# Kernel optimization log

Hardware: AMD Instinct MI355X
Metric: run time of the kernel (lower is better)

Reference implementation:

```python
import jax, jax.numpy as jnp
import numpy as np

E, TOPK = 8, 2
N_EMBD, TEXT_DIM, FULL = 1024, 1024, 1024
BS, SEQ = 8, 512

def setup_inputs() -> dict:
    key = jax.random.key(0)
    ks = jax.random.split(key, 8)
    return {
        "x": jax.random.normal(ks[0], (BS, SEQ, N_EMBD), jnp.float32),
        "dec_embeddings": jax.random.normal(ks[1], (BS, TEXT_DIM), jnp.float32),
        # router is zero-init in the module, but use small random weights so top-k is non-degenerate
        "router_w": jax.random.normal(ks[2], (E, TEXT_DIM), jnp.float32) * 0.02,
        "router_b": jnp.zeros((E,), jnp.float32),
        "w1": jax.random.normal(ks[3], (E, N_EMBD, N_EMBD), jnp.float32) * 0.02,
        "w2": jax.random.normal(ks[4], (E, N_EMBD, FULL), jnp.float32) * 0.02,
        "b1": jnp.zeros((E, 1, N_EMBD), jnp.float32),
        "b2": jnp.zeros((E, 1, FULL), jnp.float32),
    }

def reference(x, dec_embeddings, router_w, router_b, w1, w2, b1, b2):
    bs, seqlen, n_embd = x.shape
    logits = dec_embeddings @ router_w.T + router_b          # (bs, E)
    gate_probs = jax.nn.softmax(logits, axis=-1)
    topk_w, topk_idx = jax.lax.top_k(gate_probs, TOPK)       # (bs, k)
    topk_w = topk_w / jnp.sum(topk_w, axis=-1, keepdims=True)
    # dense all-expert 2-layer MLP (as written in the original)
    hidden = jax.nn.relu(jnp.einsum('bsn,enh->ebsh', x, w1) + b1[:, None])   # (E,bs,S,H)
    out_all = jnp.einsum('ebsh,ehf->ebsf', hidden, w2) + b2[:, None]          # (E,bs,S,F)
    out_b = jnp.transpose(out_all, (1, 0, 2, 3))             # (bs,E,S,F)
    # gather top-k expert outputs per batch item and combine
    sel = jnp.take_along_axis(out_b, topk_idx[:, :, None, None], axis=1)      # (bs,k,S,F)
    final_output = jnp.sum(topk_w[:, :, None, None] * sel, axis=1)            # (bs,S,F)
    combined_mask = jnp.max(jax.nn.one_hot(topk_idx, E, dtype=x.dtype), axis=1)  # (bs,E)
    aux_loss = E * jnp.sum(jnp.mean(gate_probs, axis=0) * jnp.mean(combined_mask, axis=0))
    return final_output, aux_loss, combined_mask, logits
```

## Files before the change

kernel.cpp:

```cpp
#include <hip/hip_runtime.h>
#include <hip/hip_bf16.h>
#include <stdint.h>

#define EXP 8
#define DIM 1024
#define SEQL 512
#define BATCH 8
#define OUT_FINAL_N (BATCH * SEQL * DIM)
#define OFF_AUX    4194304
#define OFF_MASK   4194305
#define OFF_LOGITS 4194369

typedef __bf16 bf16_t;
typedef bf16_t bf16x8 __attribute__((ext_vector_type(8)));
typedef bf16_t bf16x4 __attribute__((ext_vector_type(4)));
typedef float  f32x4  __attribute__((ext_vector_type(4)));

typedef __attribute__((address_space(1))) void* as1p;
typedef __attribute__((address_space(3))) void* as3p;

__device__ __forceinline__ void glds16(const void* g, void* l) {
  __builtin_amdgcn_global_load_lds((as1p)(void*)g, (as3p)l, 16, 0, 0);
}

__global__ __launch_bounds__(256) void prep_kernel(
    const float* __restrict__ x, const float* __restrict__ dec,
    const float* __restrict__ rw, const float* __restrict__ rb,
    const float* __restrict__ w1, const float* __restrict__ w2,
    bf16_t* __restrict__ xb, bf16_t* __restrict__ w1t, bf16_t* __restrict__ w2t,
    float* __restrict__ out_aux, float* __restrict__ out_mask,
    float* __restrict__ out_logits, int* __restrict__ idx_ws,
    float* __restrict__ w_ws) {
  __shared__ __align__(16) char tileb[64 * 144];
  __shared__ float part[256];
  __shared__ float lg64[64];
  __shared__ float probs[64];
  __shared__ float msk[64];
  const int bid = blockIdx.x;
  const int t = threadIdx.x;

  if (bid < 4096) {
    const int z = bid >> 8;
    const int rem = bid & 255;
    const int k0 = (rem >> 4) * 64;
    const int n0 = (rem & 15) * 64;
    const float* src = (z < 8) ? (w1 + (size_t)z * DIM * DIM)
                               : (w2 + (size_t)(z - 8) * DIM * DIM);
    bf16_t* dst = (z < 8) ? (w1t + (size_t)z * DIM * DIM)
                          : (w2t + (size_t)(z - 8) * DIM * DIM);
    const int c4 = t & 15;
    const int rr = t >> 4;
    float4 v[4];
#pragma unroll
    for (int r = 0; r < 4; ++r)
      v[r] = *(const float4*)(src + (size_t)(k0 + rr * 4 + r) * DIM + n0 + c4 * 4);
    const float* vp = (const float*)v;
#pragma unroll
    for (int c = 0; c < 4; ++c) {
      bf16x4 o;
#pragma unroll
      for (int jk = 0; jk < 4; ++jk) o[jk] = (bf16_t)vp[jk * 4 + c];
      *(bf16x4*)(tileb + (c4 * 4 + c) * 144 + rr * 8) = o;
    }
    __syncthreads();
#pragma unroll
    for (int ii = 0; ii < 2; ++ii) {
      const int n = (t >> 3) + 32 * ii;
      const int j = t & 7;
      bf16x8 vv = *(const bf16x8*)(tileb + n * 144 + j * 16);
      *(bf16x8*)(dst + (size_t)(n0 + n) * DIM + k0 + j * 8) = vv;
    }
  } else if (bid < 4096 + 512) {
    const int i0 = (bid - 4096) * 2048 + t;
    float4 v[8];
#pragma unroll
    for (int i = 0; i < 8; ++i) v[i] = ((const float4*)x)[i0 + i * 256];
#pragma unroll
    for (int i = 0; i < 8; ++i) {
      bf16x4 o;
      o[0] = (bf16_t)v[i].x; o[1] = (bf16_t)v[i].y;
      o[2] = (bf16_t)v[i].z; o[3] = (bf16_t)v[i].w;
      ((bf16x4*)xb)[i0 + i * 256] = o;
    }
  } else {
    const int p = t >> 2, seg = t & 3;
    const int b = p >> 3, e = p & 7;
    const float4* dv = (const float4*)(dec + b * DIM + seg * 256);
    const float4* wv = (const float4*)(rw + e * DIM + seg * 256);
    float s = 0.f;
#pragma unroll 8
    for (int i = 0; i < 64; ++i) {
      float4 a = dv[i], c = wv[i];
      s += a.x * c.x + a.y * c.y + a.z * c.z + a.w * c.w;
    }
    part[t] = s;
    __syncthreads();
    if (seg == 0) {
      float l = part[t] + part[t + 1] + part[t + 2] + part[t + 3] + rb[e];
      lg64[p] = l;
      out_logits[p] = l;
    }
    __syncthreads();
    if (t < 8) {
      float l[8];
      float mx = -1e30f;
#pragma unroll
      for (int k = 0; k < 8; ++k) { l[k] = lg64[t * 8 + k]; mx = fmaxf(mx, l[k]); }
      float pe[8];
      float sum = 0.f;
#pragma unroll
      for (int k = 0; k < 8; ++k) { pe[k] = expf(l[k] - mx); sum += pe[k]; }
      float inv = 1.f / sum;
#pragma unroll
      for (int k = 0; k < 8; ++k) { pe[k] *= inv; probs[t * 8 + k] = pe[k]; }
      int i0 = 0;
#pragma unroll
      for (int k = 1; k < 8; ++k) if (pe[k] > pe[i0]) i0 = k;
      int i1 = (i0 == 0) ? 1 : 0;
#pragma unroll
      for (int k = 0; k < 8; ++k) if (k != i0 && pe[k] > pe[i1]) i1 = k;
      float p0 = pe[i0], p1 = pe[i1];
      float invs = 1.f / (p0 + p1);
      idx_ws[t * 2] = i0;
      idx_ws[t * 2 + 1] = i1;
      w_ws[t * 2] = p0 * invs;
      w_ws[t * 2 + 1] = p1 * invs;
#pragma unroll
      for (int k = 0; k < 8; ++k) {
        float m = (k == i0 || k == i1) ? 1.f : 0.f;
        msk[t * 8 + k] = m;
        out_mask[t * 8 + k] = m;
      }
    }
    __syncthreads();
    if (t == 0) {
      float aux = 0.f;
#pragma unroll
      for (int k = 0; k < 8; ++k) {
        float mp = 0.f, mm = 0.f;
#pragma unroll
        for (int bb = 0; bb < 8; ++bb) { mp += probs[bb * 8 + k]; mm += msk[bb * 8 + k]; }
        aux += (mp * 0.125f) * (mm * 0.125f);
      }
      out_aux[0] = 8.f * aux;
    }
  }
}

__global__ __launch_bounds__(512, 2) void gemm1_kernel(const bf16_t* __restrict__ xb,
                                                       const bf16_t* __restrict__ w1t,
                                                       const float* __restrict__ b1,
                                                       const int* __restrict__ topk_idx,
                                                       bf16_t* __restrict__ hidden) {
  __shared__ __align__(16) char smem[73728];
  const int tid = threadIdx.x;
  const int g = tid >> 8;
  const int t = tid & 255;
  const int bN = blockIdx.x, bM = blockIdx.y, b = blockIdx.z;
  const int slot = b * 2 + g;
  const int e = topk_idx[slot];

  const bf16_t* A  = xb + ((size_t)b * SEQL + bM * 128) * DIM;
  const bf16_t* Bt = w1t + ((size_t)e * DIM + bN * 128) * DIM;

  char* sA = smem;
  char* sB = smem + 24576 + g * 24576;

  const int rlA = tid >> 2, cpA = (tid & 3) ^ (rlA & 3);
  const bf16_t* gA = A + (size_t)rlA * DIM + cpA * 8;
  const int rlB = t >> 2, cpB = (t & 3) ^ (rlB & 3);
  const bf16_t* gB0 = Bt + (size_t)rlB * DIM + cpB * 8;
  const bf16_t* gB1 = gB0 + (size_t)64 * DIM;

  const int lane = tid & 63, wg = (tid >> 6) & 3;
  const int wr = wg >> 1, wc = wg & 1;
  const int m15 = lane & 15, q = lane >> 4;
  const char* ra[4];
  const char* rb[4];
#pragma unroll
  for (int i = 0; i < 4; ++i) {
    const int r = wr * 64 + i * 16 + m15;
    ra[i] = sA + r * 64 + ((q ^ (r & 3)) * 16);
    const int n = wc * 64 + i * 16 + m15;
    rb[i] = sB + n * 64 + ((q ^ (n & 3)) * 16);
  }

  f32x4 acc[4][4];
#pragma unroll
  for (int i = 0; i < 4; ++i)
#pragma unroll
    for (int j = 0; j < 4; ++j) acc[i][j] = {0.f, 0.f, 0.f, 0.f};

  glds16(gA, sA + tid * 16);
  glds16(gB0, sB + t * 16);
  glds16(gB1, sB + 4096 + t * 16);
  glds16(gA + 32, sA + 8192 + tid * 16);
  glds16(gB0 + 32, sB + 8192 + t * 16);
  glds16(gB1 + 32, sB + 8192 + 4096 + t * 16);

  int cur = 0;
  for (int kt = 0; kt < 32; ++kt) {
    if (kt < 31) {
      asm volatile("s_waitcnt vmcnt(3)" ::: "memory");
    } else {
      asm volatile("s_waitcnt vmcnt(0)" ::: "memory");
    }
    __builtin_amdgcn_s_barrier();
    asm volatile("" ::: "memory");
    if (kt < 30) {
      int nb = cur + 2; if (nb >= 3) nb -= 3;
      const int off = (kt + 2) * 32;
      glds16(gA + off, sA + nb * 8192 + tid * 16);
      glds16(gB0 + off, sB + nb * 8192 + t * 16);
      glds16(gB1 + off, sB + nb * 8192 + 4096 + t * 16);
    }
    bf16x8 af[4], bfr[4];
#pragma unroll
    for (int i = 0; i < 4; ++i) af[i] = *(const bf16x8*)(ra[i] + cur * 8192);
#pragma unroll
    for (int j = 0; j < 4; ++j) bfr[j] = *(const bf16x8*)(rb[j] + cur * 8192);
    __builtin_amdgcn_s_setprio(1);
#pragma unroll
    for (int i = 0; i < 4; ++i)
#pragma unroll
      for (int j = 0; j < 4; ++j)
        acc[i][j] = __builtin_amdgcn_mfma_f32_16x16x32_bf16(af[i], bfr[j], acc[i][j], 0, 0, 0);
    __builtin_amdgcn_s_setprio(0);
    cur += 1; if (cur == 3) cur = 0;
  }

  __syncthreads();
  bf16_t* hb = (bf16_t*)(smem + g * 34816);
  const float* be = b1 + e * DIM;
#pragma unroll
  for (int i = 0; i < 4; ++i)
#pragma unroll
    for (int j = 0; j < 4; ++j) {
      const int colL = wc * 64 + j * 16 + m15;
      const float bias = be[bN * 128 + colL];
#pragma unroll
      for (int r = 0; r < 4; ++r) {
        const int rowL = wr * 64 + i * 16 + q * 4 + r;
        hb[rowL * 136 + colL] = (bf16_t)fmaxf(acc[i][j][r] + bias, 0.f);
      }
    }
  __syncthreads();
  bf16_t* H = hidden + (size_t)slot * SEQL * DIM + ((size_t)bM * 128) * DIM + bN * 128;
#pragma unroll
  for (int ii = 0; ii < 8; ++ii) {
    const int r = (t >> 4) + 16 * ii;
    const int c = t & 15;
    bf16x8 vv = *(const bf16x8*)(hb + r * 136 + c * 8);
    *(bf16x8*)(H + (size_t)r * DIM + c * 8) = vv;
  }
}

__global__ __launch_bounds__(512, 2) void gemm2_kernel(const bf16_t* __restrict__ hidden,
                                                       const bf16_t* __restrict__ w2t,
                                                       const float* __restrict__ b2,
                                                       const int* __restrict__ topk_idx,
                                                       const float* __restrict__ topk_w,
                                                       float* __restrict__ out) {
  __shared__ __align__(16) char smem[98304];
  const int tid = threadIdx.x;
  const int g = tid >> 8;
  const int t = tid & 255;
  const int bN = blockIdx.x, bM = blockIdx.y, b = blockIdx.z;
  const int slot = b * 2 + g;
  const int e = topk_idx[slot];
  const float sg = topk_w[slot];

  const bf16_t* A  = hidden + ((size_t)slot * SEQL + bM * 128) * DIM;
  const bf16_t* Bt = w2t + ((size_t)e * DIM + bN * 128) * DIM;

  char* sA = smem + g * 49152;
  char* sB = sA + 24576;

  const int rl = t >> 2, cp = (t & 3) ^ (rl & 3);
  const bf16_t* gA0 = A + (size_t)rl * DIM + cp * 8;
  const bf16_t* gA1 = gA0 + (size_t)64 * DIM;
  const bf16_t* gB0 = Bt + (size_t)rl * DIM + cp * 8;
  const bf16_t* gB1 = gB0 + (size_t)64 * DIM;

  const int lane = tid & 63, wg = (tid >> 6) & 3;
  const int wr = wg >> 1, wc = wg & 1;
  const int m15 = lane & 15, q = lane >> 4;
  const char* ra[4];
  const char* rb[4];
#pragma unroll
  for (int i = 0; i < 4; ++i) {
    const int r = wr * 64 + i * 16 + m15;
    ra[i] = sA + r * 64 + ((q ^ (r & 3)) * 16);
    const int n = wc * 64 + i * 16 + m15;
    rb[i] = sB + n * 64 + ((q ^ (n & 3)) * 16);
  }

  f32x4 acc[4][4];
#pragma unroll
  for (int i = 0; i < 4; ++i)
#pragma unroll
    for (int j = 0; j < 4; ++j) acc[i][j] = {0.f, 0.f, 0.f, 0.f};

  glds16(gA0, sA + t * 16);
  glds16(gA1, sA + 4096 + t * 16);
  glds16(gB0, sB + t * 16);
  glds16(gB1, sB + 4096 + t * 16);
  glds16(gA0 + 32, sA + 8192 + t * 16);
  glds16(gA1 + 32, sA + 8192 + 4096 + t * 16);
  glds16(gB0 + 32, sB + 8192 + t * 16);
  glds16(gB1 + 32, sB + 8192 + 4096 + t * 16);

  int cur = 0;
  for (int kt = 0; kt < 32; ++kt) {
    if (kt < 31) {
      asm volatile("s_waitcnt vmcnt(4)" ::: "memory");
    } else {
      asm volatile("s_waitcnt vmcnt(0)" ::: "memory");
    }
    __builtin_amdgcn_s_barrier();
    asm volatile("" ::: "memory");
    if (kt < 30) {
      int nb = cur + 2; if (nb >= 3) nb -= 3;
      const int off = (kt + 2) * 32;
      char* dA = sA + nb * 8192 + t * 16;
      char* dB = sB + nb * 8192 + t * 16;
      glds16(gA0 + off, dA);
      glds16(gA1 + off, dA + 4096);
      glds16(gB0 + off, dB);
      glds16(gB1 + off, dB + 4096);
    }
    bf16x8 af[4], bfr[4];
#pragma unroll
    for (int i = 0; i < 4; ++i) af[i] = *(const bf16x8*)(ra[i] + cur * 8192);
#pragma unroll
    for (int j = 0; j < 4; ++j) bfr[j] = *(const bf16x8*)(rb[j] + cur * 8192);
    __builtin_amdgcn_s_setprio(1);
#pragma unroll
    for (int i = 0; i < 4; ++i)
#pragma unroll
      for (int j = 0; j < 4; ++j)
        acc[i][j] = __builtin_amdgcn_mfma_f32_16x16x32_bf16(af[i], bfr[j], acc[i][j], 0, 0, 0);
    __builtin_amdgcn_s_setprio(0);
    cur += 1; if (cur == 3) cur = 0;
  }

  __syncthreads();
  float* scr = (float*)smem;
  const float w0 = topk_w[b * 2], w1v = topk_w[b * 2 + 1];
  const float* be0 = b2 + topk_idx[b * 2] * DIM;
  const float* be1 = b2 + topk_idx[b * 2 + 1] * DIM;
  float* O = out + (size_t)b * SEQL * DIM;
#pragma unroll
  for (int i = 0; i < 4; ++i) {
    if (g == 1) {
#pragma unroll
      for (int j = 0; j < 4; ++j)
#pragma unroll
        for (int r = 0; r < 4; ++r)
          scr[(j * 4 + r) * 256 + t] = sg * acc[i][j][r];
    }
    __syncthreads();
    if (g == 0) {
#pragma unroll
      for (int j = 0; j < 4; ++j) {
        const int col = bN * 128 + wc * 64 + j * 16 + m15;
        const float bb = w0 * be0[col] + w1v * be1[col];
        const int row = bM * 128 + wr * 64 + i * 16 + q * 4;
#pragma unroll
        for (int r = 0; r < 4; ++r)
          O[(size_t)(row + r) * DIM + col] =
              sg * acc[i][j][r] + scr[(j * 4 + r) * 256 + t] + bb;
      }
    }
    __syncthreads();
  }
}

extern "C" void kernel_launch(void* const* d_in, const int* in_sizes, int n_in,
                              void* d_out, int out_size, void* d_ws, size_t ws_size,
                              hipStream_t stream) {
  const float* x   = (const float*)d_in[0];
  const float* dec = (const float*)d_in[1];
  const float* rw  = (const float*)d_in[2];
  const float* rb  = (const float*)d_in[3];
  const float* w1  = (const float*)d_in[4];
  const float* w2  = (const float*)d_in[5];
  const float* b1  = (const float*)d_in[6];
  const float* b2  = (const float*)d_in[7];
  float* out = (float*)d_out;

  char* ws = (char*)d_ws;
  bf16_t* xb   = (bf16_t*)(ws);
  bf16_t* w1t  = (bf16_t*)(ws + (8u << 20));
  bf16_t* w2t  = (bf16_t*)(ws + (24u << 20));
  bf16_t* hid  = (bf16_t*)(ws + (40u << 20));
  int*    idxw = (int*)(ws + (56u << 20));
  float*  ww   = (float*)(ws + (56u << 20) + 64);

  hipLaunchKernelGGL(prep_kernel, dim3(4096 + 512 + 1), dim3(256), 0, stream,
                     x, dec, rw, rb, w1, w2, xb, w1t, w2t,
                     out + OFF_AUX, out + OFF_MASK, out + OFF_LOGITS, idxw, ww);
  hipLaunchKernelGGL(gemm1_kernel, dim3(8, 4, 8), dim3(512), 0, stream,
                     xb, w1t, b1, idxw, hid);
  hipLaunchKernelGGL(gemm2_kernel, dim3(8, 4, 8), dim3(512), 0, stream,
                     hid, w2t, b2, idxw, ww, out);
}
```

Baseline: 192.7 us.

## Pipeline weight transpose across four k-tiles and double gemm1 K-step to 64

The weight transpose/convert blocks now each handle four 64-row k-tiles, using two LDS buffers so global loads of the next tile overlap the shared-memory transpose and store of the current one. This cuts the block count from 4096 to 1024. gemm1 moves from a 32-wide to a 64-wide K tile with a wider XOR swizzle, halving the number of barriers and main-loop iterations. In exchange it doubles LDS use to 144KB per block, which lowers occupancy and may conflict with the 2-blocks-per-CU launch bound.

```diff
diff --git a/kernel.cpp b/kernel.cpp
--- a/kernel.cpp
+++ b/kernel.cpp
@@ -31,7 +31,7 @@
     float* __restrict__ out_aux, float* __restrict__ out_mask,
     float* __restrict__ out_logits, int* __restrict__ idx_ws,
     float* __restrict__ w_ws) {
-  __shared__ __align__(16) char tileb[64 * 144];
+  __shared__ __align__(16) char tb[2][9216];
   __shared__ float part[256];
   __shared__ float lg64[64];
   __shared__ float probs[64];
@@ -39,10 +39,10 @@
   const int bid = blockIdx.x;
   const int t = threadIdx.x;
 
-  if (bid < 4096) {
-    const int z = bid >> 8;
-    const int rem = bid & 255;
-    const int k0 = (rem >> 4) * 64;
+  if (bid < 1024) {
+    const int z = bid >> 6;
+    const int rem = bid & 63;
+    const int kbase = (rem >> 4) * 256;
     const int n0 = (rem & 15) * 64;
     const float* src = (z < 8) ? (w1 + (size_t)z * DIM * DIM)
                                : (w2 + (size_t)(z - 8) * DIM * DIM);
@@ -50,28 +50,59 @@
                           : (w2t + (size_t)(z - 8) * DIM * DIM);
     const int c4 = t & 15;
     const int rr = t >> 4;
-    float4 v[4];
-#pragma unroll
-    for (int r = 0; r < 4; ++r)
-      v[r] = *(const float4*)(src + (size_t)(k0 + rr * 4 + r) * DIM + n0 + c4 * 4);
-    const float* vp = (const float*)v;
-#pragma unroll
-    for (int c = 0; c < 4; ++c) {
-      bf16x4 o;
-#pragma unroll
-      for (int jk = 0; jk < 4; ++jk) o[jk] = (bf16_t)vp[jk * 4 + c];
-      *(bf16x4*)(tileb + (c4 * 4 + c) * 144 + rr * 8) = o;
-    }
-    __syncthreads();
-#pragma unroll
-    for (int ii = 0; ii < 2; ++ii) {
-      const int n = (t >> 3) + 32 * ii;
-      const int j = t & 7;
-      bf16x8 vv = *(const bf16x8*)(tileb + n * 144 + j * 16);
-      *(bf16x8*)(dst + (size_t)(n0 + n) * DIM + k0 + j * 8) = vv;
-    }
-  } else if (bid < 4096 + 512) {
-    const int i0 = (bid - 4096) * 2048 + t;
+
+    auto LOAD = [&](float4* v, int k0) {
+#pragma unroll
+      for (int r = 0; r < 4; ++r)
+        v[r] = *(const float4*)(src + (size_t)(k0 + rr * 4 + r) * DIM + n0 + c4 * 4);
+    };
+    auto WRITE = [&](const float4* v, char* buf) {
+      const float* vp = (const float*)v;
+#pragma unroll
+      for (int c = 0; c < 4; ++c) {
+        bf16x4 o;
+#pragma unroll
+        for (int jk = 0; jk < 4; ++jk) o[jk] = (bf16_t)vp[jk * 4 + c];
+        *(bf16x4*)(buf + (c4 * 4 + c) * 144 + rr * 8) = o;
+      }
+    };
+    auto RDSTORE = [&](const char* buf, int k0) {
+#pragma unroll
+      for (int ii = 0; ii < 2; ++ii) {
+        const int n = (t >> 3) + 32 * ii;
+        const int j = t & 7;
+        bf16x8 vv = *(const bf16x8*)(buf + n * 144 + j * 16);
+        *(bf16x8*)(dst + (size_t)(n0 + n) * DIM + k0 + j * 8) = vv;
+      }
+    };
+
+    float4 va[4], vb[4];
+    LOAD(va, kbase);
+    LOAD(vb, kbase + 64);
+    WRITE(va, tb[0]);
+    LOAD(va, kbase + 128);
+    asm volatile("s_waitcnt lgkmcnt(0)" ::: "memory");
+    __builtin_amdgcn_s_barrier();
+    asm volatile("" ::: "memory");
+    RDSTORE(tb[0], kbase);
+    WRITE(vb, tb[1]);
+    LOAD(vb, kbase + 192);
+    asm volatile("s_waitcnt lgkmcnt(0)" ::: "memory");
+    __builtin_amdgcn_s_barrier();
+    asm volatile("" ::: "memory");
+    RDSTORE(tb[1], kbase + 64);
+    WRITE(va, tb[0]);
+    asm volatile("s_waitcnt lgkmcnt(0)" ::: "memory");
+    __builtin_amdgcn_s_barrier();
+    asm volatile("" ::: "memory");
+    RDSTORE(tb[0], kbase + 128);
+    WRITE(vb, tb[1]);
+    asm volatile("s_waitcnt lgkmcnt(0)" ::: "memory");
+    __builtin_amdgcn_s_barrier();
+    asm volatile("" ::: "memory");
+    RDSTORE(tb[1], kbase + 192);
+  } else if (bid < 1024 + 512) {
+    const int i0 = (bid - 1024) * 2048 + t;
     float4 v[8];
 #pragma unroll
     for (int i = 0; i < 8; ++i) v[i] = ((const float4*)x)[i0 + i * 256];
@@ -152,7 +183,7 @@
                                                        const float* __restrict__ b1,
                                                        const int* __restrict__ topk_idx,
                                                        bf16_t* __restrict__ hidden) {
-  __shared__ __align__(16) char smem[73728];
+  __shared__ __align__(16) char smem[147456];
   const int tid = threadIdx.x;
   const int g = tid >> 8;
   const int t = tid & 255;
@@ -164,25 +195,29 @@
   const bf16_t* Bt = w1t + ((size_t)e * DIM + bN * 128) * DIM;
 
   char* sA = smem;
-  char* sB = smem + 24576 + g * 24576;
-
-  const int rlA = tid >> 2, cpA = (tid & 3) ^ (rlA & 3);
-  const bf16_t* gA = A + (size_t)rlA * DIM + cpA * 8;
-  const int rlB = t >> 2, cpB = (t & 3) ^ (rlB & 3);
-  const bf16_t* gB0 = Bt + (size_t)rlB * DIM + cpB * 8;
-  const bf16_t* gB1 = gB0 + (size_t)64 * DIM;
+  char* sB = smem + 49152 + g * 49152;
+
+  const int cpA = (tid & 7) ^ ((tid >> 3) & 7);
+  const bf16_t* gA0 = A + (size_t)(tid >> 3) * DIM + cpA * 8;
+  const bf16_t* gA1 = gA0 + (size_t)64 * DIM;
+  const int cpB = (t & 7) ^ ((t >> 3) & 7);
+  const bf16_t* gB0 = Bt + (size_t)(t >> 3) * DIM + cpB * 8;
+  const bf16_t* gB1 = gB0 + (size_t)32 * DIM;
+  const bf16_t* gB2 = gB0 + (size_t)64 * DIM;
+  const bf16_t* gB3 = gB0 + (size_t)96 * DIM;
 
   const int lane = tid & 63, wg = (tid >> 6) & 3;
   const int wr = wg >> 1, wc = wg & 1;
   const int m15 = lane & 15, q = lane >> 4;
-  const char* ra[4];
-  const char* rb[4];
+  int aoff[4], boff[4];
 #pragma unroll
   for (int i = 0; i < 4; ++i) {
     const int r = wr * 64 + i * 16 + m15;
-    ra[i] = sA + r * 64 + ((q ^ (r & 3)) * 16);
+    const int sr = r & 7;
+    aoff[i] = r * 128 + ((q ^ (sr & 3)) + ((sr >> 2) << 2)) * 16;
     const int n = wc * 64 + i * 16 + m15;
-    rb[i] = sB + n * 64 + ((q ^ (n & 3)) * 16);
+    const int sn = n & 7;
+    boff[i] = n * 128 + ((q ^ (sn & 3)) + ((sn >> 2) << 2)) * 16;
   }
 
   f32x4 acc[4][4];
@@ -191,41 +226,51 @@
 #pragma unroll
     for (int j = 0; j < 4; ++j) acc[i][j] = {0.f, 0.f, 0.f, 0.f};
 
-  glds16(gA, sA + tid * 16);
-  glds16(gB0, sB + t * 16);
-  glds16(gB1, sB + 4096 + t * 16);
-  glds16(gA + 32, sA + 8192 + tid * 16);
-  glds16(gB0 + 32, sB + 8192 + t * 16);
-  glds16(gB1 + 32, sB + 8192 + 4096 + t * 16);
-
+  auto STAGE = [&](int kt, int nb) {
+    const int off = kt * 64;
+    char* dA = sA + nb * 16384;
+    glds16(gA0 + off, dA + tid * 16);
+    glds16(gA1 + off, dA + 8192 + tid * 16);
+    char* dB = sB + nb * 16384 + t * 16;
+    glds16(gB0 + off, dB);
+    glds16(gB1 + off, dB + 4096);
+    glds16(gB2 + off, dB + 8192);
+    glds16(gB3 + off, dB + 12288);
+  };
+
+  STAGE(0, 0);
+  STAGE(1, 1);
   int cur = 0;
-  for (int kt = 0; kt < 32; ++kt) {
-    if (kt < 31) {
-      asm volatile("s_waitcnt vmcnt(3)" ::: "memory");
+  for (int kt = 0; kt < 16; ++kt) {
+    if (kt < 15) {
+      asm volatile("s_waitcnt vmcnt(6)" ::: "memory");
     } else {
       asm volatile("s_waitcnt vmcnt(0)" ::: "memory");
     }
     __builtin_amdgcn_s_barrier();
     asm volatile("" ::: "memory");
-    if (kt < 30) {
+    if (kt < 14) {
       int nb = cur + 2; if (nb >= 3) nb -= 3;
-      const int off = (kt + 2) * 32;
-      glds16(gA + off, sA + nb * 8192 + tid * 16);
-      glds16(gB0 + off, sB + nb * 8192 + t * 16);
-      glds16(gB1 + off, sB + nb * 8192 + 4096 + t * 16);
-    }
-    bf16x8 af[4], bfr[4];
-#pragma unroll
-    for (int i = 0; i < 4; ++i) af[i] = *(const bf16x8*)(ra[i] + cur * 8192);
-#pragma unroll
-    for (int j = 0; j < 4; ++j) bfr[j] = *(const bf16x8*)(rb[j] + cur * 8192);
-    __builtin_amdgcn_s_setprio(1);
-#pragma unroll
-    for (int i = 0; i < 4; ++i)
-#pragma unroll
-      for (int j = 0; j < 4; ++j)
-        acc[i][j] = __builtin_amdgcn_mfma_f32_16x16x32_bf16(af[i], bfr[j], acc[i][j], 0, 0, 0);
-    __builtin_amdgcn_s_setprio(0);
+      STAGE(kt + 2, nb);
+    }
+    const char* bA = sA + cur * 16384;
+    const char* bB = sB + cur * 16384;
+#pragma unroll
+    for (int ks = 0; ks < 2; ++ks) {
+      bf16x8 af[4], bfr[4];
+#pragma unroll
+      for (int i = 0; i < 4; ++i) af[i] = *(const bf16x8*)(bA + (aoff[i] ^ (ks << 6)));
+#pragma unroll
+      for (int j = 0; j < 4; ++j) bfr[j] = *(const bf16x8*)(bB + (boff[j] ^ (ks << 6)));
+      __builtin_amdgcn_s_setprio(1);
+#pragma unroll
+      for (int i = 0; i < 4; ++i)
+#pragma unroll
+        for (int j = 0; j < 4; ++j)
+          acc[i][j] = __builtin_amdgcn_mfma_f32_16x16x32_bf16(af[i], bfr[j], acc[i][j], 0, 0, 0);
+      __builtin_amdgcn_s_setprio(0);
+    }
+    __builtin_amdgcn_sched_barrier(0);
     cur += 1; if (cur == 3) cur = 0;
   }
 
@@ -397,7 +442,7 @@
   int*    idxw = (int*)(ws + (56u << 20));
   float*  ww   = (float*)(ws + (56u << 20) + 64);
 
-  hipLaunchKernelGGL(prep_kernel, dim3(4096 + 512 + 1), dim3(256), 0, stream,
+  hipLaunchKernelGGL(prep_kernel, dim3(1024 + 512 + 1), dim3(256), 0, stream,
                      x, dec, rw, rb, w1, w2, xb, w1t, w2t,
                      out + OFF_AUX, out + OFF_MASK, out + OFF_LOGITS, idxw, ww);
   hipLaunchKernelGGL(gemm1_kernel, dim3(8, 4, 8), dim3(512), 0, stream,
```

Result: no change. 196.0 us (+1.7%).

## Move w2 bf16 transpose-convert into gemm1 launch to overlap with GEMM

Applied to the files above, without the earlier changes.

The w2 fp32-to-bf16 transpose is moved out of the prep kernel and into extra blocks of the gemm1 launch, which now uses a flat 1D grid of 256 GEMM blocks plus 1024 conversion blocks, each conversion block handling two tiles. The aim is to overlap the memory-bound w2 conversion with the compute-bound first GEMM and shorten the prep kernel. The risk is that conversion blocks compete with GEMM blocks for CUs and bandwidth, and that the 1024 extra 512-thread blocks reserve the large shared-memory allocation, which may limit occupancy.

```diff
diff --git a/kernel.cpp b/kernel.cpp
--- a/kernel.cpp
+++ b/kernel.cpp
@@ -31,7 +31,7 @@
     float* __restrict__ out_aux, float* __restrict__ out_mask,
     float* __restrict__ out_logits, int* __restrict__ idx_ws,
     float* __restrict__ w_ws) {
-  __shared__ __align__(16) char tileb[64 * 144];
+  __shared__ __align__(16) char tileb[9216];
   __shared__ float part[256];
   __shared__ float lg64[64];
   __shared__ float probs[64];
@@ -39,15 +39,13 @@
   const int bid = blockIdx.x;
   const int t = threadIdx.x;
 
-  if (bid < 4096) {
+  if (bid < 2048) {
     const int z = bid >> 8;
     const int rem = bid & 255;
     const int k0 = (rem >> 4) * 64;
     const int n0 = (rem & 15) * 64;
-    const float* src = (z < 8) ? (w1 + (size_t)z * DIM * DIM)
-                               : (w2 + (size_t)(z - 8) * DIM * DIM);
-    bf16_t* dst = (z < 8) ? (w1t + (size_t)z * DIM * DIM)
-                          : (w2t + (size_t)(z - 8) * DIM * DIM);
+    const float* src = w1 + (size_t)z * DIM * DIM;
+    bf16_t* dst = w1t + (size_t)z * DIM * DIM;
     const int c4 = t & 15;
     const int rr = t >> 4;
     float4 v[4];
@@ -70,8 +68,8 @@
       bf16x8 vv = *(const bf16x8*)(tileb + n * 144 + j * 16);
       *(bf16x8*)(dst + (size_t)(n0 + n) * DIM + k0 + j * 8) = vv;
     }
-  } else if (bid < 4096 + 512) {
-    const int i0 = (bid - 4096) * 2048 + t;
+  } else if (bid < 2048 + 512) {
+    const int i0 = (bid - 2048) * 2048 + t;
     float4 v[8];
 #pragma unroll
     for (int i = 0; i < 8; ++i) v[i] = ((const float4*)x)[i0 + i * 256];
@@ -151,12 +149,52 @@
                                                        const bf16_t* __restrict__ w1t,
                                                        const float* __restrict__ b1,
                                                        const int* __restrict__ topk_idx,
-                                                       bf16_t* __restrict__ hidden) {
+                                                       bf16_t* __restrict__ hidden,
+                                                       const float* __restrict__ w2,
+                                                       bf16_t* __restrict__ w2t) {
   __shared__ __align__(16) char smem[73728];
+  const int bid = blockIdx.x;
   const int tid = threadIdx.x;
+
+  if (bid >= 256) {
+    const int half = tid >> 8;
+    const int tt = tid & 255;
+    char* tb = smem + half * 9216;
+    const int tile = (bid - 256) * 2 + half;
+    const int z = tile >> 8;
+    const int rem = tile & 255;
+    const int k0 = (rem >> 4) * 64;
+    const int n0 = (rem & 15) * 64;
+    const float* src = w2 + (size_t)z * DIM * DIM;
+    bf16_t* dst = w2t + (size_t)z * DIM * DIM;
+    const int c4 = tt & 15;
+    const int rr = tt >> 4;
+    float4 v[4];
+#pragma unroll
+    for (int r = 0; r < 4; ++r)
+      v[r] = *(const float4*)(src + (size_t)(k0 + rr * 4 + r) * DIM + n0 + c4 * 4);
+    const float* vp = (const float*)v;
+#pragma unroll
+    for (int c = 0; c < 4; ++c) {
+      bf16x4 o;
+#pragma unroll
+      for (int jk = 0; jk < 4; ++jk) o[jk] = (bf16_t)vp[jk * 4 + c];
+      *(bf16x4*)(tb + (c4 * 4 + c) * 144 + rr * 8) = o;
+    }
+    __syncthreads();
+#pragma unroll
+    for (int ii = 0; ii < 2; ++ii) {
+      const int n = (tt >> 3) + 32 * ii;
+      const int j = tt & 7;
+      bf16x8 vv = *(const bf16x8*)(tb + n * 144 + j * 16);
+      *(bf16x8*)(dst + (size_t)(n0 + n) * DIM + k0 + j * 8) = vv;
+    }
+    return;
+  }
+
+  const int bN = bid & 7, bM = (bid >> 3) & 3, b = bid >> 5;
   const int g = tid >> 8;
   const int t = tid & 255;
-  const int bN = blockIdx.x, bM = blockIdx.y, b = blockIdx.z;
   const int slot = b * 2 + g;
   const int e = topk_idx[slot];
 
@@ -397,11 +435,11 @@
   int*    idxw = (int*)(ws + (56u << 20));
   float*  ww   = (float*)(ws + (56u << 20) + 64);
 
-  hipLaunchKernelGGL(prep_kernel, dim3(4096 + 512 + 1), dim3(256), 0, stream,
+  hipLaunchKernelGGL(prep_kernel, dim3(2048 + 512 + 1), dim3(256), 0, stream,
                      x, dec, rw, rb, w1, w2, xb, w1t, w2t,
                      out + OFF_AUX, out + OFF_MASK, out + OFF_LOGITS, idxw, ww);
-  hipLaunchKernelGGL(gemm1_kernel, dim3(8, 4, 8), dim3(512), 0, stream,
-                     xb, w1t, b1, idxw, hid);
+  hipLaunchKernelGGL(gemm1_kernel, dim3(256 + 1024), dim3(512), 0, stream,
+                     xb, w1t, b1, idxw, hid, w2, w2t);
   hipLaunchKernelGGL(gemm2_kernel, dim3(8, 4, 8), dim3(512), 0, stream,
                      hid, w2t, b2, idxw, ww, out);
 }
```

Result: no change. 196.5 us (+2.0%).
